# Kernel optimization log

Measured on AMD Instinct MI355X. Metric: run time of the kernel, lower is better.

## Reference

```python
import jax, jax.numpy as jnp
import numpy as np

# static config matching init_kwargs
IN_SIZE = 128
OUT_SIZE = 128
KSIZE = 3
POS = 10
DIL = 1
B = 8
L = 8192


def setup_inputs() -> dict:
    key = jax.random.key(0)
    k1, k2, k3, k4, k5 = jax.random.split(key, 5)
    inputs = jax.random.normal(k1, (B, IN_SIZE, L), dtype=jnp.float32)
    connections = jax.random.randint(k2, (B, L), 0, L)  # indices into length axis
    mask = jax.random.randint(k3, (B, L), 0, 2).astype(bool)
    ch_in = (2 * IN_SIZE + POS) * KSIZE  # 798
    W = jax.random.normal(k4, (OUT_SIZE, ch_in), dtype=jnp.float32) / np.float32(np.sqrt(ch_in))
    b = jax.random.normal(k5, (OUT_SIZE,), dtype=jnp.float32) * 0.01
    return {"inputs": inputs, "connections": connections, "mask": mask, "W": W, "b": b}


def reference(inputs, connections, mask, W, b):
    Bn, C, Ln = inputs.shape
    # gather neighbor features: out[b,c,l] = inputs[b,c,connections[b,l]]  -> [B,C,L]
    conn_vals = jnp.take_along_axis(inputs, connections[:, None, :], axis=2)
    # trig positional encoding of relative offsets  -> [B,POS,L]
    pos = jnp.arange(Ln, dtype=jnp.float32)[None]              # [1,L]
    delta = (pos - connections.astype(jnp.float32))[:, None, :]  # [B,1,L]
    scales = (2.0 ** jnp.arange(POS, dtype=jnp.float32))[None, :, None]
    penc = jnp.sin(scales * delta / 1000.0)
    out = jnp.concatenate([inputs, conn_vals, penc], axis=1)   # [B, 2C+POS, L]
    # non-causal pad + unfold (window KSIZE, step 1); num windows == L
    pad = KSIZE * DIL // 2
    out = jnp.pad(out, ((0, 0), (0, 0), (pad, pad)))
    # build [B, Ch, KSIZE, L]: window k is out_padded[..., k : k+L]
    out = jnp.stack([out[..., k:k + Ln] for k in range(KSIZE)], axis=2)
    out = out.reshape(Bn, -1, Ln)                               # [B, Ch*KSIZE, L]
    # 1x1 conv == per-position GEMM
    y = jnp.einsum('oc,bcl->bol', W, out) + b[None, :, None]    # [B, OUT, L]
    return y * mask[:, None, :].astype(y.dtype)
```

## Files before the change

### kernel.cpp

```cpp
#include <hip/hip_runtime.h>
#include <math.h>

#define B_    8
#define C_    128
#define L_    8192
#define O_    128
#define POS_  10
#define CHIN  798
#define CH_   266
#define GSTR  128
#define NCH   9
#define TL2   128
#define G_ELEMS  ((size_t)B_ * L_ * GSTR)
#define WT_ELEMS ((size_t)3 * NCH * O_ * 32)

typedef _Float16 half8 __attribute__((ext_vector_type(8)));
typedef short short8 __attribute__((ext_vector_type(8)));
typedef float f32x4  __attribute__((ext_vector_type(4)));

__device__ __forceinline__ void detect_core(const uint4* __restrict__ m,
                                            int* __restrict__ mflag, int tid) {
    __shared__ int s[2];
    if (tid < 2) s[tid] = 0;
    __syncthreads();
    unsigned sub = 0, mid = 0;
    #pragma unroll
    for (int k = 0; k < 16; ++k) {
        uint4 w = m[tid + k * 256];
        sub |= (w.x | w.y | w.z | w.w) & 0xFFFFFF00u;
        mid |= (w.y | w.w) & 0x000000FFu;
    }
    unsigned long long bs = __ballot(sub != 0);
    unsigned long long bm = __ballot(mid != 0);
    if ((tid & 63) == 0) {
        if (bs) atomicOr(&s[0], 1);
        if (bm) atomicOr(&s[1], 1);
    }
    __syncthreads();
    if (tid == 0) mflag[0] = s[0] ? 1 : (s[1] ? 0 : 2);
}

__global__ void detect_kernel(const uint4* __restrict__ m, int* __restrict__ mflag) {
    detect_core(m, mflag, threadIdx.x);
}

__global__ __launch_bounds__(256, 4)
void prep_kernel(const float* __restrict__ inputs, const float* __restrict__ W,
                 const uint4* __restrict__ maskv,
                 _Float16* __restrict__ G, _Float16* __restrict__ Wt2,
                 int* __restrict__ mflag) {
    __shared__ float tile[64][65];
    const int bid = blockIdx.x;
    const int tid = threadIdx.x;

    if (bid == 2480) { detect_core(maskv, mflag, tid); return; }

    if (bid >= 2048) {
        int idx = (bid - 2048) * 256 + tid;
        int cc  = idx & 31;
        int o   = (idx >> 5) & 127;
        int tch = idx >> 12;
        int ch  = tch % 9;
        int t   = tch / 9;
        int cg  = ch * 32 + cc;
        Wt2[idx] = (cg < CH_) ? (_Float16)W[o * CHIN + 3 * cg + t] : (_Float16)0.f;
        return;
    }

    const int b  = bid & 7;
    const int r  = bid >> 3;
    const int c0 = (r & 1) * 64;
    const int l0 = (r >> 1) * 64;
    const int ty = tid >> 6, tx = tid & 63;

    #pragma unroll
    for (int it = 0; it < 16; ++it) {
        int cl = it * 4 + ty;
        tile[cl][tx] = inputs[((size_t)(b * C_ + c0 + cl)) * L_ + l0 + tx];
    }
    __syncthreads();
    const int cp = (tid & 31) * 2;
    const int lr = tid >> 5;
    #pragma unroll
    for (int it = 0; it < 8; ++it) {
        int ll = it * 8 + lr;
        _Float16 pair[2] = {(_Float16)tile[cp][ll], (_Float16)tile[cp + 1][ll]};
        *(unsigned*)&G[((size_t)(b * L_ + l0 + ll)) * GSTR + c0 + cp] = *(unsigned*)pair;
    }
}

__global__ __launch_bounds__(256)
void k2_gemm(const _Float16* __restrict__ G, const _Float16* __restrict__ Wt2,
             const int* __restrict__ conn,
             const unsigned char* __restrict__ mask,
             const float* __restrict__ bias,
             float* __restrict__ out,
             const int* __restrict__ mflag_p) {
    __shared__ _Float16 Bs[2][132][40];
    __shared__ int conn_s[130];

    const int bid = blockIdx.x;
    const int b   = bid & 7;
    const int l0  = (bid >> 3) * TL2;
    const int tid  = threadIdx.x;
    const int wave = tid >> 6;
    const int lane = tid & 63;
    const int wo = wave & 1;
    const int wl = wave >> 1;
    const int g  = lane >> 4;
    const int ln = lane & 15;

    const _Float16* gb = G + (size_t)b * L_ * GSTR;

    for (int j = tid; j < TL2 + 2; j += 256) {
        int l_ = l0 - 1 + j;
        conn_s[j] = ((unsigned)l_ < (unsigned)L_) ? conn[b * L_ + l_] : 0;
    }

    auto bload = [&](int ch, int q) -> short8 {
        int cb = q & 3, j = q >> 2;
        int l_ = l0 - 1 + j;
        short8 v = (short8)0;
        if ((unsigned)l_ < (unsigned)L_) {
            if (ch < 4) {
                v = *(const short8*)&gb[(size_t)l_ * GSTR + ch * 32 + cb * 8];
            } else if (ch < 8) {
                int cj = conn_s[j];
                v = *(const short8*)&gb[(size_t)cj * GSTR + (ch - 4) * 32 + cb * 8];
            } else if (cb < 2) {
                float d = (float)(l_ - conn_s[j]);
                _Float16 h[8];
                #pragma unroll
                for (int e = 0; e < 8; ++e) {
                    int p = cb * 8 + e;
                    h[e] = (p < POS_) ? (_Float16)sinf(((float)(1 << p)) * d / 1000.0f)
                                      : (_Float16)0.f;
                }
                v = *(short8*)h;
            }
        }
        return v;
    };
    auto bwrite = [&](short8 s, int q, int buf) {
        int cb = q & 3, j = q >> 2;
        *(short8*)&Bs[buf][j][cb * 8] = s;
    };

#define ALOADR(DST, CH) { _Pragma("unroll") for (int t_ = 0; t_ < 3; ++t_) \
        _Pragma("unroll") for (int m_ = 0; m_ < 4; ++m_) \
            DST[t_][m_] = *(const half8*)&Wt2[((size_t)((t_ * NCH + (CH)) * O_ + wo * 64 + m_ * 16 + ln)) * 32 + g * 8]; }

#define BLOADR(CH) { s0 = bload((CH), tid); s1 = bload((CH), tid + 256); \
        if (tid < 8) s2 = bload((CH), 512 + tid); }

#define BWR(BUF) { bwrite(s0, tid, (BUF)); bwrite(s1, tid + 256, (BUF)); \
        if (tid < 8) bwrite(s2, 512 + tid, (BUF)); }

#define COMPUTE(AUSE, BUF) { _Pragma("unroll") for (int t_ = 0; t_ < 3; ++t_) { \
        half8 bf_[4]; \
        _Pragma("unroll") for (int n_ = 0; n_ < 4; ++n_) \
            bf_[n_] = *(const half8*)&Bs[BUF][wl * 64 + n_ * 16 + ln + t_][8 * g]; \
        _Pragma("unroll") for (int m_ = 0; m_ < 4; ++m_) \
            _Pragma("unroll") for (int n_ = 0; n_ < 4; ++n_) \
                acc[m_][n_] = __builtin_amdgcn_mfma_f32_16x16x32_f16(AUSE[t_][m_], bf_[n_], acc[m_][n_], 0, 0, 0); } }

    f32x4 acc[4][4];
    #pragma unroll
    for (int m = 0; m < 4; ++m)
        #pragma unroll
        for (int n = 0; n < 4; ++n) acc[m][n] = (f32x4)0.f;

    half8 A0[3][4], A1[3][4];
    short8 s0, s1, s2;

    ALOADR(A0, 0);
    BLOADR(0);
    BWR(0);
    __syncthreads();

    for (int ch = 0; ch < 8; ch += 2) {
        ALOADR(A1, ch + 1);
        BLOADR(ch + 1);
        COMPUTE(A0, 0);
        BWR(1);
        __syncthreads();

        ALOADR(A0, ch + 2);
        BLOADR(ch + 2);
        COMPUTE(A1, 1);
        BWR(0);
        __syncthreads();
    }
    COMPUTE(A0, 0);

    const int mflag = mflag_p[0];
    float mv[4];
    #pragma unroll
    for (int n = 0; n < 4; ++n) {
        int l = l0 + wl * 64 + n * 16 + ln;
        int idx = b * L_ + l;
        if (mflag == 1)      mv[n] = mask[idx] ? 1.f : 0.f;
        else if (mflag == 0) mv[n] = ((const int*)mask)[idx] ? 1.f : 0.f;
        else                 mv[n] = ((const int*)mask)[2 * idx] ? 1.f : 0.f;
    }
    #pragma unroll
    for (int m = 0; m < 4; ++m) {
        #pragma unroll
        for (int r = 0; r < 4; ++r) {
            int o = wo * 64 + m * 16 + g * 4 + r;
            float bo = bias[o];
            #pragma unroll
            for (int n = 0; n < 4; ++n) {
                int l = l0 + wl * 64 + n * 16 + ln;
                out[((size_t)(b * O_ + o)) * L_ + l] = (acc[m][n][r] + bo) * mv[n];
            }
        }
    }
#undef ALOADR
#undef BLOADR
#undef BWR
#undef COMPUTE
}

__global__ __launch_bounds__(256, 2)
void cc_fallback_kernel(const float* __restrict__ inputs,
                        const int* __restrict__ conn,
                        const unsigned char* __restrict__ mask,
                        const float* __restrict__ W,
                        const float* __restrict__ bias,
                        float* __restrict__ out,
                        const int* __restrict__ mflag_p) {
    __shared__ int   conn_s[130];
    __shared__ float feat_s[16][132];
    __shared__ float Ws[48][136];

    const int b   = blockIdx.y;
    const int l0  = blockIdx.x * 128;
    const int tid = threadIdx.x;
    const int ot  = tid >> 4;
    const int lt  = tid & 15;
    const int o0  = ot * 8;
    const int ll  = lt * 8;

    for (int j = tid; j < 130; j += 256) {
        int lg = l0 - 1 + j;
        conn_s[j] = ((unsigned)lg < (unsigned)L_) ? conn[b * L_ + lg] : -1;
    }
    float acc[8][8];
    #pragma unroll
    for (int i = 0; i < 8; ++i)
        #pragma unroll
        for (int j = 0; j < 8; ++j) acc[i][j] = 0.f;

    const int tc = ot, tj = lt;
    for (int chunk = 0; chunk < 17; ++chunk) {
        const int CN  = (chunk < 16) ? 16 : POS_;
        const int cg0 = chunk * 16;
        const int col0 = 3 * cg0;
        __syncthreads();
        {
            const int nw = O_ * CN * 3;
            for (int idx = tid; idx < nw; idx += 256) {
                int o = idx & 127, kk = idx >> 7;
                Ws[kk][o] = W[o * CHIN + col0 + kk];
            }
        }
        if (chunk < 8) {
            const float* src = inputs + ((size_t)b * C_ + (cg0 + tc)) * L_;
            for (int j = tj; j < 130; j += 16) {
                int lg = l0 - 1 + j;
                feat_s[tc][j] = ((unsigned)lg < (unsigned)L_) ? src[lg] : 0.f;
            }
        } else if (chunk < 16) {
            const float* src = inputs + ((size_t)b * C_ + (cg0 - 128 + tc)) * L_;
            for (int j = tj; j < 130; j += 16) {
                int cj = conn_s[j];
                feat_s[tc][j] = (cj >= 0) ? src[cj] : 0.f;
            }
        } else if (tc < POS_) {
            const float sc = (float)(1 << tc);
            for (int j = tj; j < 130; j += 16) {
                int cj = conn_s[j];
                int lg = l0 - 1 + j;
                float v = 0.f;
                if (cj >= 0) v = sinf((sc * (float)(lg - cj)) / 1000.0f);
                feat_s[tc][j] = v;
            }
        }
        __syncthreads();
        for (int c = 0; c < CN; ++c) {
            float f[10];
            float4 fa = *(const float4*)&feat_s[c][ll];
            float4 fb = *(const float4*)&feat_s[c][ll + 4];
            float2 fc2 = *(const float2*)&feat_s[c][ll + 8];
            f[0]=fa.x; f[1]=fa.y; f[2]=fa.z; f[3]=fa.w;
            f[4]=fb.x; f[5]=fb.y; f[6]=fb.z; f[7]=fb.w;
            f[8]=fc2.x; f[9]=fc2.y;
            #pragma unroll
            for (int k = 0; k < 3; ++k) {
                const float* wrow = &Ws[c * 3 + k][o0];
                float4 wa = *(const float4*)&wrow[0];
                float4 wb = *(const float4*)&wrow[4];
                float w[8] = {wa.x, wa.y, wa.z, wa.w, wb.x, wb.y, wb.z, wb.w};
                #pragma unroll
                for (int oi = 0; oi < 8; ++oi)
                    #pragma unroll
                    for (int li = 0; li < 8; ++li)
                        acc[oi][li] = fmaf(w[oi], f[li + k], acc[oi][li]);
            }
        }
    }
    const int mflag = mflag_p[0];
    const int lbase = l0 + ll;
    float mv[8];
    #pragma unroll
    for (int li = 0; li < 8; ++li) {
        int idx = b * L_ + lbase + li;
        if (mflag == 1)      mv[li] = mask[idx] ? 1.f : 0.f;
        else if (mflag == 0) mv[li] = ((const int*)mask)[idx] ? 1.f : 0.f;
        else                 mv[li] = ((const int*)mask)[2 * idx] ? 1.f : 0.f;
    }
    #pragma unroll
    for (int oi = 0; oi < 8; ++oi) {
        float bo = bias[o0 + oi];
        float* dst = out + ((size_t)b * O_ + o0 + oi) * L_ + lbase;
        #pragma unroll
        for (int li = 0; li < 8; ++li) dst[li] = (acc[oi][li] + bo) * mv[li];
    }
}

extern "C" void kernel_launch(void* const* d_in, const int* in_sizes, int n_in,
                              void* d_out, int out_size, void* d_ws, size_t ws_size,
                              hipStream_t stream) {
    const float*         inputs = (const float*)d_in[0];
    const int*           conn   = (const int*)d_in[1];
    const unsigned char* mask   = (const unsigned char*)d_in[2];
    const float*         W      = (const float*)d_in[3];
    const float*         bias   = (const float*)d_in[4];
    float*               out    = (float*)d_out;

    const size_t g_bytes  = G_ELEMS * sizeof(_Float16);
    const size_t wt_bytes = WT_ELEMS * sizeof(_Float16);
    const size_t need     = g_bytes + wt_bytes + 64;

    if (ws_size < need) {
        int* mflag = (int*)d_ws;
        detect_kernel<<<1, 256, 0, stream>>>((const uint4*)mask, mflag);
        dim3 grid(L_ / 128, B_);
        cc_fallback_kernel<<<grid, 256, 0, stream>>>(inputs, conn, mask, W, bias, out, mflag);
        return;
    }

    _Float16* G     = (_Float16*)d_ws;
    _Float16* Wt2   = (_Float16*)((char*)d_ws + g_bytes);
    int*      mflag = (int*)((char*)d_ws + g_bytes + wt_bytes);

    prep_kernel<<<2481, 256, 0, stream>>>(inputs, W, (const uint4*)mask, G, Wt2, mflag);
    k2_gemm<<<512, 256, 0, stream>>>(G, Wt2, conn, mask, bias, out, mflag);
}
```

Measured before the change: 49.35 us.

## Stage weight tiles through double-buffered LDS instead of per-wave register loads

Weight (A) fragments were previously loaded straight from global memory into registers by each wave, so waves sharing an output half fetched the same data redundantly. They are now loaded cooperatively into a double-buffered shared-memory tile and read from LDS during the MFMA loop. This cuts duplicate global traffic and the register pressure of holding two full A fragment sets. In exchange it adds about 53 KB of LDS, which may lower occupancy, plus extra LDS writes and reads per chunk.

```diff
diff --git a/kernel.cpp b/kernel.cpp
--- a/kernel.cpp
+++ b/kernel.cpp
@@ -96,7 +96,8 @@
              const float* __restrict__ bias,
              float* __restrict__ out,
              const int* __restrict__ mflag_p) {
-    __shared__ _Float16 Bs[2][132][40];
+    __shared__ _Float16 As[2][128][104];
+    __shared__ _Float16 Bs[2][130][40];
     __shared__ int conn_s[130];
 
     const int bid = blockIdx.x;
@@ -117,7 +118,11 @@
         conn_s[j] = ((unsigned)l_ < (unsigned)L_) ? conn[b * L_ + l_] : 0;
     }
 
-    auto bload = [&](int ch, int q) -> short8 {
+    auto aloadg = [&](int ch, int q) -> short8 {
+        int cb = q & 3, o = (q >> 2) & 127, tp = q >> 9;
+        return *(const short8*)&Wt2[((size_t)((tp * NCH + ch) * O_ + o)) * 32 + cb * 8];
+    };
+    auto bloadg = [&](int ch, int q) -> short8 {
         int cb = q & 3, j = q >> 2;
         int l_ = l0 - 1 + j;
         short8 v = (short8)0;
@@ -141,28 +146,35 @@
         }
         return v;
     };
-    auto bwrite = [&](short8 s, int q, int buf) {
-        int cb = q & 3, j = q >> 2;
-        *(short8*)&Bs[buf][j][cb * 8] = s;
-    };
-
-#define ALOADR(DST, CH) { _Pragma("unroll") for (int t_ = 0; t_ < 3; ++t_) \
-        _Pragma("unroll") for (int m_ = 0; m_ < 4; ++m_) \
-            DST[t_][m_] = *(const half8*)&Wt2[((size_t)((t_ * NCH + (CH)) * O_ + wo * 64 + m_ * 16 + ln)) * 32 + g * 8]; }
-
-#define BLOADR(CH) { s0 = bload((CH), tid); s1 = bload((CH), tid + 256); \
-        if (tid < 8) s2 = bload((CH), 512 + tid); }
-
-#define BWR(BUF) { bwrite(s0, tid, (BUF)); bwrite(s1, tid + 256, (BUF)); \
-        if (tid < 8) bwrite(s2, 512 + tid, (BUF)); }
-
-#define COMPUTE(AUSE, BUF) { _Pragma("unroll") for (int t_ = 0; t_ < 3; ++t_) { \
+
+#define ALOADG(CH) { a0 = aloadg((CH), tid);        a1 = aloadg((CH), tid + 256); \
+                     a2 = aloadg((CH), tid + 512);  a3 = aloadg((CH), tid + 768); \
+                     a4 = aloadg((CH), tid + 1024); a5 = aloadg((CH), tid + 1280); }
+
+#define AWR1(V, Q, BUF) { int cb_ = (Q) & 3, o_ = ((Q) >> 2) & 127, tp_ = (Q) >> 9; \
+        *(short8*)&As[BUF][o_][tp_ * 32 + cb_ * 8] = V; }
+
+#define AWR(BUF) { AWR1(a0, tid, BUF) AWR1(a1, tid + 256, BUF) \
+                   AWR1(a2, tid + 512, BUF) AWR1(a3, tid + 768, BUF) \
+                   AWR1(a4, tid + 1024, BUF) AWR1(a5, tid + 1280, BUF) }
+
+#define BLOADG(CH) { s0 = bloadg((CH), tid); s1 = bloadg((CH), tid + 256); \
+        if (tid < 8) s2 = bloadg((CH), 512 + tid); }
+
+#define BWR1(V, Q, BUF) { int cb_ = (Q) & 3, j_ = (Q) >> 2; \
+        *(short8*)&Bs[BUF][j_][cb_ * 8] = V; }
+
+#define BWR(BUF) { BWR1(s0, tid, BUF) BWR1(s1, tid + 256, BUF) \
+        if (tid < 8) { BWR1(s2, 512 + tid, BUF) } }
+
+#define COMPUTE(BUF) { _Pragma("unroll") for (int t_ = 0; t_ < 3; ++t_) { \
         half8 bf_[4]; \
         _Pragma("unroll") for (int n_ = 0; n_ < 4; ++n_) \
             bf_[n_] = *(const half8*)&Bs[BUF][wl * 64 + n_ * 16 + ln + t_][8 * g]; \
-        _Pragma("unroll") for (int m_ = 0; m_ < 4; ++m_) \
+        _Pragma("unroll") for (int m_ = 0; m_ < 4; ++m_) { \
+            half8 af_ = *(const half8*)&As[BUF][wo * 64 + m_ * 16 + ln][t_ * 32 + 8 * g]; \
             _Pragma("unroll") for (int n_ = 0; n_ < 4; ++n_) \
-                acc[m_][n_] = __builtin_amdgcn_mfma_f32_16x16x32_f16(AUSE[t_][m_], bf_[n_], acc[m_][n_], 0, 0, 0); } }
+                acc[m_][n_] = __builtin_amdgcn_mfma_f32_16x16x32_f16(af_, bf_[n_], acc[m_][n_], 0, 0, 0); } } }
 
     f32x4 acc[4][4];
     #pragma unroll
@@ -170,28 +182,24 @@
         #pragma unroll
         for (int n = 0; n < 4; ++n) acc[m][n] = (f32x4)0.f;
 
-    half8 A0[3][4], A1[3][4];
-    short8 s0, s1, s2;
-
-    ALOADR(A0, 0);
-    BLOADR(0);
-    BWR(0);
+    short8 a0, a1, a2, a3, a4, a5, s0, s1, s2;
+
+    ALOADG(0); BLOADG(0);
+    AWR(0); BWR(0);
     __syncthreads();
 
     for (int ch = 0; ch < 8; ch += 2) {
-        ALOADR(A1, ch + 1);
-        BLOADR(ch + 1);
-        COMPUTE(A0, 0);
-        BWR(1);
+        ALOADG(ch + 1); BLOADG(ch + 1);
+        COMPUTE(0);
+        AWR(1); BWR(1);
         __syncthreads();
 
-        ALOADR(A0, ch + 2);
-        BLOADR(ch + 2);
-        COMPUTE(A1, 1);
-        BWR(0);
+        ALOADG(ch + 2); BLOADG(ch + 2);
+        COMPUTE(1);
+        AWR(0); BWR(0);
         __syncthreads();
     }
-    COMPUTE(A0, 0);
+    COMPUTE(0);
 
     const int mflag = mflag_p[0];
     float mv[4];
@@ -216,8 +224,11 @@
             }
         }
     }
-#undef ALOADR
-#undef BLOADR
+#undef ALOADG
+#undef AWR1
+#undef AWR
+#undef BLOADG
+#undef BWR1
 #undef BWR
 #undef COMPUTE
 }
```

Measured after the change: 45.24 us. -8.3%, faster.
